# Performance work log

Hardware: AMD Instinct MI355X
Metric: run time of the kernel (lower is better)

Reference implementation:

```python
import jax, jax.numpy as jnp
import numpy as np

D_MODEL = 1024
NUM_HEADS = 16
HEAD_DIM = D_MODEL // NUM_HEADS


def setup_inputs() -> dict:
    key = jax.random.key(0)
    ks = jax.random.split(key, 9)
    s = 1.0 / np.sqrt(D_MODEL)
    x = jax.random.normal(ks[0], (2, 2048, D_MODEL), dtype=jnp.float32)
    Wq = jax.random.normal(ks[1], (D_MODEL, D_MODEL), dtype=jnp.float32) * s
    Wk = jax.random.normal(ks[2], (D_MODEL, D_MODEL), dtype=jnp.float32) * s
    Wv = jax.random.normal(ks[3], (D_MODEL, D_MODEL), dtype=jnp.float32) * s
    Wo = jax.random.normal(ks[4], (D_MODEL, D_MODEL), dtype=jnp.float32) * s
    bq = jax.random.normal(ks[5], (D_MODEL,), dtype=jnp.float32) * s
    bk = jax.random.normal(ks[6], (D_MODEL,), dtype=jnp.float32) * s
    bv = jax.random.normal(ks[7], (D_MODEL,), dtype=jnp.float32) * s
    bo = jax.random.normal(ks[8], (D_MODEL,), dtype=jnp.float32) * s
    return {"x": x, "Wq": Wq, "bq": bq, "Wk": Wk, "bk": bk, "Wv": Wv, "bv": bv, "Wo": Wo, "bo": bo}


def reference(x, Wq, bq, Wk, bk, Wv, bv, Wo, bo):
    B, S, D = x.shape
    H, Hd = NUM_HEADS, HEAD_DIM
    # QKV projections
    q = (x @ Wq + bq).reshape(B, S, H, Hd).transpose(0, 2, 1, 3)  # [B,H,S,Hd]
    k = (x @ Wk + bk).reshape(B, S, H, Hd).transpose(0, 2, 1, 3)
    v = (x @ Wv + bv).reshape(B, S, H, Hd).transpose(0, 2, 1, 3)
    scores = jnp.einsum("bhqd,bhkd->bhqk", q, k) / jnp.sqrt(jnp.float32(Hd))
    attn = jax.nn.softmax(scores, axis=-1)
    out = jnp.einsum("bhqk,bhkd->bhqd", attn, v)  # [B,H,S,Hd]
    out = out.transpose(0, 2, 1, 3).reshape(B, S, D)
    return out @ Wo + bo
```

## Files before the change

### kernel.cpp

```cpp
#include <hip/hip_runtime.h>
#include <hip/hip_bf16.h>


typedef unsigned short u16;

#define D_MODEL 1024
#define NHEAD 16
#define HDIM 64
#define BATCH 2
#define SEQ 2048
#define MTOT (BATCH * SEQ)

#define QSCALE 0.18033688011112042f

using frag_ab = __attribute__((ext_vector_type(8))) short;
using frag_cd = __attribute__((ext_vector_type(4))) float;

__device__ __forceinline__ u16 f2u(float f) {
    union { float f; unsigned int i; } x;
    x.f = f;
    unsigned int r = x.i + 0x7fffu + ((x.i >> 16) & 1u);
    return (u16)(r >> 16);
}
__device__ __forceinline__ u16 f2u_fast(float f) {
    union { float f; unsigned int i; } x;
    x.f = f;
    return (u16)((x.i + 0x8000u) >> 16);
}

__global__ void prep(const float* __restrict__ W0, const float* __restrict__ W1,
                     const float* __restrict__ W2, const float* __restrict__ W3,
                     const float* __restrict__ X, u16* __restrict__ Wt,
                     u16* __restrict__ Xb) {
    const int z = blockIdx.z;
    const int tx = threadIdx.x, ty = threadIdx.y;
    if (z < 4) {
        __shared__ u16 t[32][33];
        const float* W = (z == 0) ? W0 : (z == 1) ? W1 : (z == 2) ? W2 : W3;
        u16* o = Wt + (size_t)z * D_MODEL * D_MODEL;
        int n0 = blockIdx.x * 32, k0 = blockIdx.y * 32;
        #pragma unroll
        for (int i = ty; i < 32; i += 8) t[i][tx] = f2u(W[(size_t)(k0 + i) * D_MODEL + n0 + tx]);
        __syncthreads();
        #pragma unroll
        for (int i = ty; i < 32; i += 8) o[(size_t)(n0 + i) * D_MODEL + k0 + tx] = t[tx][i];
    } else {
        int tid = ty * 32 + tx;
        size_t base = ((size_t)(blockIdx.y * 32 + blockIdx.x) * 256 + tid) * 16;
        #pragma unroll
        for (int c = 0; c < 4; ++c) {
            float4 v = *(const float4*)&X[base + c * 4];
            ushort4 o;
            o.x = f2u(v.x); o.y = f2u(v.y); o.z = f2u(v.z); o.w = f2u(v.w);
            *(ushort4*)&Xb[base + c * 4] = o;
        }
    }
}

__launch_bounds__(256, 3)
__global__ void gemm_qkvt(const u16* __restrict__ xb, const u16* __restrict__ Wt,
                          const float* __restrict__ bq, const float* __restrict__ bk,
                          const float* __restrict__ bv, u16* __restrict__ QKw,
                          u16* __restrict__ Vtw) {
    constexpr int BK = 64;
    __shared__ __attribute__((aligned(16))) u16 As[128 * BK];
    __shared__ __attribute__((aligned(16))) u16 Bs[128 * BK];

    const int tid = threadIdx.x;
    const int w = tid >> 6;
    const int lane = tid & 63;
    const int lrow = lane & 15, lquad = lane >> 4;
    const size_t WSZ = (size_t)D_MODEL * D_MODEL;

    const int bid = blockIdx.x;
    const bool vt = bid >= 512;
    const int z = vt ? 2 : (bid >> 8);
    const int t = vt ? (bid - 512) : (bid & 255);
    const int n0 = vt ? (t & 31) * 128 : (t & 7) * 128;
    const int m0 = vt ? (t >> 5) * 128 : (t >> 3) * 128;
    const u16* Ap = vt ? (Wt + 2 * WSZ) : xb;
    const u16* Bp = vt ? xb : (Wt + (size_t)z * WSZ);
    const float* bias = vt ? bv : (z ? bk : bq);

    frag_cd acc[4][4];
    #pragma unroll
    for (int i = 0; i < 4; i++)
        #pragma unroll
        for (int j = 0; j < 4; j++) acc[i][j] = (frag_cd){0.f, 0.f, 0.f, 0.f};

    const int wm = (w >> 1) * 64, wn = (w & 1) * 64;

    for (int k0 = 0; k0 < D_MODEL; k0 += BK) {
        __syncthreads();
        #pragma unroll
        for (int it = 0; it < 4; ++it) {
            int c = it * 256 + tid;
            int r = c >> 3, c8 = c & 7;
            const u16* ga = Ap + (size_t)(m0 + r) * D_MODEL + k0 + c8 * 8;
            char* la = (char*)As + (it * 256 + w * 64) * 16;
            __builtin_amdgcn_global_load_lds((const __attribute__((address_space(1))) void*)ga,
                                             (__attribute__((address_space(3))) void*)la, 16, 0, 0);
            const u16* gb = Bp + (size_t)(n0 + r) * D_MODEL + k0 + c8 * 8;
            char* lb = (char*)Bs + (it * 256 + w * 64) * 16;
            __builtin_amdgcn_global_load_lds((const __attribute__((address_space(1))) void*)gb,
                                             (__attribute__((address_space(3))) void*)lb, 16, 0, 0);
        }
        __syncthreads();

        #pragma unroll
        for (int kc = 0; kc < 2; ++kc) {
            frag_ab av[4], bvv[4];
            #pragma unroll
            for (int i = 0; i < 4; i++)
                av[i] = *(const frag_ab*)&As[(wm + i * 16 + lrow) * BK + kc * 32 + lquad * 8];
            #pragma unroll
            for (int j = 0; j < 4; j++)
                bvv[j] = *(const frag_ab*)&Bs[(wn + j * 16 + lrow) * BK + kc * 32 + lquad * 8];
            #pragma unroll
            for (int i = 0; i < 4; i++)
                #pragma unroll
                for (int j = 0; j < 4; j++)
                    acc[i][j] = __builtin_amdgcn_mfma_f32_16x16x32_bf16(av[i], bvv[j], acc[i][j], 0, 0, 0);
        }
    }

    const float scale = (!vt && z == 0) ? QSCALE : 1.0f;
    #pragma unroll
    for (int j = 0; j < 4; j++) {
        int gn = n0 + wn + j * 16 + lrow;
        #pragma unroll
        for (int i = 0; i < 4; i++) {
            #pragma unroll
            for (int rr = 0; rr < 4; ++rr) {
                int gm = m0 + wm + i * 16 + lquad * 4 + rr;
                if (!vt) {
                    float v = (acc[i][j][rr] + bias[gn]) * scale;
                    u16* oz = QKw + (size_t)z * ((size_t)MTOT * D_MODEL);
                    int b = gm >> 11, s = gm & (SEQ - 1);
                    int h = gn >> 6, d = gn & (HDIM - 1);
                    oz[(((size_t)(b * NHEAD + h)) * SEQ + s) * HDIM + d] = f2u(v);
                } else {
                    float v = acc[i][j][rr] + bias[gm];
                    int h = gm >> 6, d = gm & (HDIM - 1);
                    int b = gn >> 11, s = gn & (SEQ - 1);
                    Vtw[(((size_t)(b * NHEAD + h)) * HDIM + d) * SEQ + s] = f2u(v);
                }
            }
        }
    }
}

__launch_bounds__(256, 2)
__global__ void gemm_out(const u16* __restrict__ A, const u16* __restrict__ Wt,
                         const float* __restrict__ bias, float* __restrict__ out) {
    constexpr int BK = 64;
    __shared__ __attribute__((aligned(16))) u16 As[64 * BK];
    __shared__ __attribute__((aligned(16))) u16 Bs[128 * BK];

    const int tid = threadIdx.x;
    const int w = tid >> 6;
    const int lane = tid & 63;
    const int lrow = lane & 15, lquad = lane >> 4;
    const int m0 = blockIdx.y * 64, n0 = blockIdx.x * 128;

    frag_cd acc[2][4];
    #pragma unroll
    for (int i = 0; i < 2; i++)
        #pragma unroll
        for (int j = 0; j < 4; j++) acc[i][j] = (frag_cd){0.f, 0.f, 0.f, 0.f};

    const int wm = (w >> 1) * 32, wn = (w & 1) * 64;

    for (int k0 = 0; k0 < D_MODEL; k0 += BK) {
        __syncthreads();
        #pragma unroll
        for (int it = 0; it < 2; ++it) {
            int c = it * 256 + tid;
            int r = c >> 3, c8 = c & 7;
            const u16* ga = A + (size_t)(m0 + r) * D_MODEL + k0 + c8 * 8;
            char* la = (char*)As + (it * 256 + w * 64) * 16;
            __builtin_amdgcn_global_load_lds((const __attribute__((address_space(1))) void*)ga,
                                             (__attribute__((address_space(3))) void*)la, 16, 0, 0);
        }
        #pragma unroll
        for (int it = 0; it < 4; ++it) {
            int c = it * 256 + tid;
            int r = c >> 3, c8 = c & 7;
            const u16* gb = Wt + (size_t)(n0 + r) * D_MODEL + k0 + c8 * 8;
            char* lb = (char*)Bs + (it * 256 + w * 64) * 16;
            __builtin_amdgcn_global_load_lds((const __attribute__((address_space(1))) void*)gb,
                                             (__attribute__((address_space(3))) void*)lb, 16, 0, 0);
        }
        __syncthreads();

        #pragma unroll
        for (int kc = 0; kc < 2; ++kc) {
            frag_ab av[2], bvv[4];
            #pragma unroll
            for (int i = 0; i < 2; i++)
                av[i] = *(const frag_ab*)&As[(wm + i * 16 + lrow) * BK + kc * 32 + lquad * 8];
            #pragma unroll
            for (int j = 0; j < 4; j++)
                bvv[j] = *(const frag_ab*)&Bs[(wn + j * 16 + lrow) * BK + kc * 32 + lquad * 8];
            #pragma unroll
            for (int i = 0; i < 2; i++)
                #pragma unroll
                for (int j = 0; j < 4; j++)
                    acc[i][j] = __builtin_amdgcn_mfma_f32_16x16x32_bf16(av[i], bvv[j], acc[i][j], 0, 0, 0);
        }
    }

    #pragma unroll
    for (int j = 0; j < 4; j++) {
        int gn = n0 + wn + j * 16 + lrow;
        float bvf = bias[gn];
        #pragma unroll
        for (int i = 0; i < 2; i++)
            #pragma unroll
            for (int rr = 0; rr < 4; ++rr) {
                int gm = m0 + wm + i * 16 + lquad * 4 + rr;
                out[(size_t)gm * D_MODEL + gn] = acc[i][j][rr] + bvf;
            }
    }
}

__launch_bounds__(512, 4)
__global__ void attn_kernel(const u16* __restrict__ Q, const u16* __restrict__ K,
                            const u16* __restrict__ Vt, u16* __restrict__ O) {
    constexpr int SKK = 72;
    constexpr int SKV = 136;
    __shared__ __attribute__((aligned(16))) u16 Ks[128 * SKK];
    __shared__ __attribute__((aligned(16))) u16 Vs[64 * SKV];
    __shared__ __attribute__((aligned(16))) u16 Ps[8 * 16 * SKV];

    const int tid = threadIdx.x;
    const int w = tid >> 6;
    const int lane = tid & 63;
    const int lrow = lane & 15, lquad = lane >> 4;
    const int bh = blockIdx.y;
    const int q0 = blockIdx.x * 128;
    const size_t base = (size_t)bh * SEQ * HDIM;
    const u16* Qg = Q + base;
    const u16* Kg = K + base;
    const u16* Vg = Vt + base;

    frag_ab qf[2];
    #pragma unroll
    for (int kc = 0; kc < 2; ++kc)
        qf[kc] = *(const frag_ab*)&Qg[(size_t)(q0 + w * 16 + lrow) * HDIM + kc * 32 + lquad * 8];

    frag_cd accO[4], lacc;
    lacc = (frag_cd){0.f, 0.f, 0.f, 0.f};
    #pragma unroll
    for (int df = 0; df < 4; df++) accO[df] = (frag_cd){0.f, 0.f, 0.f, 0.f};
    frag_ab ones;
    #pragma unroll
    for (int t = 0; t < 8; ++t) ones[t] = (short)0x3F80;

    u16* Pw = Ps + w * 16 * SKV;

    for (int kt = 0; kt < SEQ / 128; ++kt) {
        __syncthreads();
        #pragma unroll
        for (int it = 0; it < 2; ++it) {
            int c = it * 512 + tid;
            int rk = c >> 3, ck = (c & 7) * 8;
            *(uint4*)&Ks[rk * SKK + ck] = *(const uint4*)&Kg[(size_t)(kt * 128 + rk) * HDIM + ck];
            int rv = c >> 4, cv = (c & 15) * 8;
            *(uint4*)&Vs[rv * SKV + cv] = *(const uint4*)&Vg[(size_t)rv * SEQ + kt * 128 + cv];
        }
        __syncthreads();

        frag_cd sc[8];
        #pragma unroll
        for (int nf = 0; nf < 8; nf++) sc[nf] = (frag_cd){0.f, 0.f, 0.f, 0.f};
        #pragma unroll
        for (int kc = 0; kc < 2; ++kc) {
            #pragma unroll
            for (int nf = 0; nf < 8; nf++) {
                frag_ab kf = *(const frag_ab*)&Ks[(nf * 16 + lrow) * SKK + kc * 32 + lquad * 8];
                sc[nf] = __builtin_amdgcn_mfma_f32_16x16x32_bf16(qf[kc], kf, sc[nf], 0, 0, 0);
            }
        }

        #pragma unroll
        for (int nf = 0; nf < 8; nf++)
            #pragma unroll
            for (int i = 0; i < 4; i++)
                Pw[(lquad * 4 + i) * SKV + nf * 16 + lrow] = f2u_fast(exp2f(sc[nf][i]));

        #pragma unroll
        for (int kc = 0; kc < 4; ++kc) {
            frag_ab pf = *(const frag_ab*)&Pw[lrow * SKV + kc * 32 + lquad * 8];
            lacc = __builtin_amdgcn_mfma_f32_16x16x32_bf16(pf, ones, lacc, 0, 0, 0);
            #pragma unroll
            for (int df = 0; df < 4; df++) {
                frag_ab vf = *(const frag_ab*)&Vs[(df * 16 + lrow) * SKV + kc * 32 + lquad * 8];
                accO[df] = __builtin_amdgcn_mfma_f32_16x16x32_bf16(pf, vf, accO[df], 0, 0, 0);
            }
        }
    }

    const int b = bh >> 4, h = bh & (NHEAD - 1);
    #pragma unroll
    for (int df = 0; df < 4; df++)
        #pragma unroll
        for (int i = 0; i < 4; i++) {
            int s = q0 + w * 16 + lquad * 4 + i;
            int d = df * 16 + lrow;
            O[((size_t)(b * SEQ + s)) * D_MODEL + h * HDIM + d] = f2u(accO[df][i] / lacc[i]);
        }
}

extern "C" void kernel_launch(void* const* d_in, const int* in_sizes, int n_in,
                              void* d_out, int out_size, void* d_ws, size_t ws_size,
                              hipStream_t stream) {
    const float* x  = (const float*)d_in[0];
    const float* Wq = (const float*)d_in[1];
    const float* bq = (const float*)d_in[2];
    const float* Wk = (const float*)d_in[3];
    const float* bk = (const float*)d_in[4];
    const float* Wv = (const float*)d_in[5];
    const float* bv = (const float*)d_in[6];
    const float* Wo = (const float*)d_in[7];
    const float* bo = (const float*)d_in[8];

    u16* ws = (u16*)d_ws;
    const size_t WSZ = (size_t)D_MODEL * D_MODEL;
    const size_t TSZ = (size_t)MTOT * D_MODEL;
    u16* xb  = ws;
    u16* Wt  = ws + 4 * WSZ;
    u16* QKw = ws + 8 * WSZ;
    u16* Vtw = QKw + 2 * TSZ;
    u16* Aw  = Vtw + TSZ;

    prep<<<dim3(32, 32, 5), dim3(32, 8), 0, stream>>>(Wq, Wk, Wv, Wo, x, Wt, xb);
    gemm_qkvt<<<dim3(768), 256, 0, stream>>>(xb, Wt, bq, bk, bv, QKw, Vtw);
    attn_kernel<<<dim3(16, 32), 512, 0, stream>>>(QKw, QKw + TSZ, Vtw, Aw);
    gemm_out<<<dim3(8, 64), 256, 0, stream>>>(Aw, Wt + 3 * WSZ, bo, (float*)d_out);
}
```

Before: 223.1 us.

## Keep attention probabilities in registers via transposed S=K·Qᵀ MFMA layout

Computes the score tile transposed (K as A operand, Q as B), so each lane's exp'd probabilities already sit in the B-operand layout of a 16x16x16 bf16 MFMA for the PV product. The per-warp shared-memory P buffer, its store/reload round trip and the ones-matrix MFMA for row sums all go away; row sums now come from a register reduction with two cross-lane shuffles. The output is accumulated transposed and written as packed 4-element stores. The trade-off is twice as many MFMAs of half the K depth (16x16x16 instead of 16x16x32) and narrower 8-byte V reads from shared memory.

```diff
diff --git a/kernel.cpp b/kernel.cpp
--- a/kernel.cpp
+++ b/kernel.cpp
@@ -14,6 +14,7 @@
 #define QSCALE 0.18033688011112042f
 
 using frag_ab = __attribute__((ext_vector_type(8))) short;
+using frag_s4 = __attribute__((ext_vector_type(4))) short;
 using frag_cd = __attribute__((ext_vector_type(4))) float;
 
 __device__ __forceinline__ u16 f2u(float f) {
@@ -22,10 +23,10 @@
     unsigned int r = x.i + 0x7fffu + ((x.i >> 16) & 1u);
     return (u16)(r >> 16);
 }
-__device__ __forceinline__ u16 f2u_fast(float f) {
-    union { float f; unsigned int i; } x;
-    x.f = f;
-    return (u16)((x.i + 0x8000u) >> 16);
+__device__ __forceinline__ unsigned int pk2(float a, float b) {
+    union { float f; unsigned int i; } x, y;
+    x.f = a; y.f = b;
+    return ((x.i + 0x8000u) >> 16) | (((y.i + 0x8000u) >> 16) << 16);
 }
 
 __global__ void prep(const float* __restrict__ W0, const float* __restrict__ W1,
@@ -231,7 +232,6 @@
     constexpr int SKV = 136;
     __shared__ __attribute__((aligned(16))) u16 Ks[128 * SKK];
     __shared__ __attribute__((aligned(16))) u16 Vs[64 * SKV];
-    __shared__ __attribute__((aligned(16))) u16 Ps[8 * 16 * SKV];
 
     const int tid = threadIdx.x;
     const int w = tid >> 6;
@@ -249,15 +249,10 @@
     for (int kc = 0; kc < 2; ++kc)
         qf[kc] = *(const frag_ab*)&Qg[(size_t)(q0 + w * 16 + lrow) * HDIM + kc * 32 + lquad * 8];
 
-    frag_cd accO[4], lacc;
-    lacc = (frag_cd){0.f, 0.f, 0.f, 0.f};
-    #pragma unroll
-    for (int df = 0; df < 4; df++) accO[df] = (frag_cd){0.f, 0.f, 0.f, 0.f};
-    frag_ab ones;
-    #pragma unroll
-    for (int t = 0; t < 8; ++t) ones[t] = (short)0x3F80;
-
-    u16* Pw = Ps + w * 16 * SKV;
+    frag_cd accOT[4];
+    #pragma unroll
+    for (int df = 0; df < 4; df++) accOT[df] = (frag_cd){0.f, 0.f, 0.f, 0.f};
+    float lacc = 0.f;
 
     for (int kt = 0; kt < SEQ / 128; ++kt) {
         __syncthreads();
@@ -273,43 +268,53 @@
 
         frag_cd sc[8];
         #pragma unroll
-        for (int nf = 0; nf < 8; nf++) sc[nf] = (frag_cd){0.f, 0.f, 0.f, 0.f};
-        #pragma unroll
-        for (int kc = 0; kc < 2; ++kc) {
-            #pragma unroll
-            for (int nf = 0; nf < 8; nf++) {
-                frag_ab kf = *(const frag_ab*)&Ks[(nf * 16 + lrow) * SKK + kc * 32 + lquad * 8];
-                sc[nf] = __builtin_amdgcn_mfma_f32_16x16x32_bf16(qf[kc], kf, sc[nf], 0, 0, 0);
+        for (int mf = 0; mf < 8; mf++) sc[mf] = (frag_cd){0.f, 0.f, 0.f, 0.f};
+        #pragma unroll
+        for (int kc = 0; kc < 2; ++kc)
+            #pragma unroll
+            for (int mf = 0; mf < 8; mf++) {
+                frag_ab kf = *(const frag_ab*)&Ks[(mf * 16 + lrow) * SKK + kc * 32 + lquad * 8];
+                sc[mf] = __builtin_amdgcn_mfma_f32_16x16x32_bf16(kf, qf[kc], sc[mf], 0, 0, 0);
             }
-        }
-
-        #pragma unroll
-        for (int nf = 0; nf < 8; nf++)
-            #pragma unroll
-            for (int i = 0; i < 4; i++)
-                Pw[(lquad * 4 + i) * SKV + nf * 16 + lrow] = f2u_fast(exp2f(sc[nf][i]));
-
-        #pragma unroll
-        for (int kc = 0; kc < 4; ++kc) {
-            frag_ab pf = *(const frag_ab*)&Pw[lrow * SKV + kc * 32 + lquad * 8];
-            lacc = __builtin_amdgcn_mfma_f32_16x16x32_bf16(pf, ones, lacc, 0, 0, 0);
+
+        frag_s4 pk[8];
+        float rs = 0.f;
+        #pragma unroll
+        for (int mf = 0; mf < 8; mf++) {
+            float e0 = exp2f(sc[mf][0]), e1 = exp2f(sc[mf][1]);
+            float e2 = exp2f(sc[mf][2]), e3 = exp2f(sc[mf][3]);
+            rs += (e0 + e1) + (e2 + e3);
+            union { frag_s4 s; unsigned int u[2]; } pu;
+            pu.u[0] = pk2(e0, e1);
+            pu.u[1] = pk2(e2, e3);
+            pk[mf] = pu.s;
+        }
+        rs += __shfl_xor(rs, 16);
+        rs += __shfl_xor(rs, 32);
+        lacc += rs;
+
+        #pragma unroll
+        for (int mf = 0; mf < 8; mf++)
             #pragma unroll
             for (int df = 0; df < 4; df++) {
-                frag_ab vf = *(const frag_ab*)&Vs[(df * 16 + lrow) * SKV + kc * 32 + lquad * 8];
-                accO[df] = __builtin_amdgcn_mfma_f32_16x16x32_bf16(pf, vf, accO[df], 0, 0, 0);
+                frag_s4 vf = *(const frag_s4*)&Vs[(df * 16 + lrow) * SKV + mf * 16 + lquad * 4];
+                accOT[df] = __builtin_amdgcn_mfma_f32_16x16x16bf16_1k(vf, pk[mf], accOT[df], 0, 0, 0);
             }
-        }
     }
 
     const int b = bh >> 4, h = bh & (NHEAD - 1);
-    #pragma unroll
-    for (int df = 0; df < 4; df++)
-        #pragma unroll
-        for (int i = 0; i < 4; i++) {
-            int s = q0 + w * 16 + lquad * 4 + i;
-            int d = df * 16 + lrow;
-            O[((size_t)(b * SEQ + s)) * D_MODEL + h * HDIM + d] = f2u(accO[df][i] / lacc[i]);
-        }
+    const int s = q0 + w * 16 + lrow;
+    const float inv = 1.0f / lacc;
+    u16* orow = O + ((size_t)(b * SEQ + s)) * D_MODEL + h * HDIM;
+    #pragma unroll
+    for (int df = 0; df < 4; df++) {
+        ushort4 o;
+        o.x = f2u(accOT[df][0] * inv);
+        o.y = f2u(accOT[df][1] * inv);
+        o.z = f2u(accOT[df][2] * inv);
+        o.w = f2u(accOT[df][3] * inv);
+        *(ushort4*)&orow[df * 16 + lquad * 4] = o;
+    }
 }
 
 extern "C" void kernel_launch(void* const* d_in, const int* in_sizes, int n_in,
```

New measurement: 221.5 us. No clear change (-0.7%).
